# Performance work log

Hardware: AMD Instinct MI355X
Metric: run time of the kernel (lower is better)

Reference implementation:

```python
import jax, jax.numpy as jnp
import numpy as np

B, L, D, M = 8, 4096, 512, 64


def setup_inputs() -> dict:
    key = jax.random.key(0)
    k1, k2, k3 = jax.random.split(key, 3)
    scale = 1.0 / (D * D)
    return {
        "q": jax.random.normal(k1, (B, L, D), dtype=jnp.float32),
        "w_real": scale * jax.random.normal(k2, (D, D, M), dtype=jnp.float32),
        "w_imag": scale * jax.random.normal(k3, (D, D, M), dtype=jnp.float32),
    }


def reference(q, w_real, w_imag):
    # q: [B, L, D]; weights: [D, D, modes]
    b, l, d = q.shape
    n_freq = l // 2 + 1
    q_ft = jnp.fft.rfft(q, axis=1)                      # [B, n_freq, D] complex64
    m = min(w_real.shape[-1], n_freq)
    W = w_real[..., :m] + 1j * w_imag[..., :m]          # [D, E, m] complex
    # Batched over modes: replaces the per-mode python loop with one einsum.
    out_m = jnp.einsum('bmd,dem->bme', q_ft[:, :m, :], W)  # [B, m, D]
    out_ft = jnp.zeros((b, n_freq, d), dtype=q_ft.dtype).at[:, :m, :].set(out_m)
    return jnp.fft.irfft(out_ft, n=l, axis=1)           # [B, L, D] float32
```

## Files before the change

### kernel.cpp

```cpp
#include <hip/hip_runtime.h>

#define B_ 8
#define L_ 4096
#define D_ 512
#define M_ 64

typedef __attribute__((ext_vector_type(8))) short bh8;
typedef __attribute__((ext_vector_type(4))) float f4;
typedef __attribute__((ext_vector_type(4))) unsigned u32x4;

__device__ inline unsigned short f2bf(float f) {
  unsigned u = __float_as_uint(f);
  return (unsigned short)((u + 0x7fffu + ((u >> 16) & 1u)) >> 16);
}
__device__ inline unsigned packbf(float lo, float hi) {
  return (unsigned)f2bf(lo) | ((unsigned)f2bf(hi) << 16);
}

__device__ __forceinline__ void gl16(const float* g, void* l) {
  __builtin_amdgcn_global_load_lds(
      (const __attribute__((address_space(1))) unsigned*)g,
      (__attribute__((address_space(3))) unsigned*)l, 16, 0, 0);
}

__global__ void k_ftab(unsigned short* __restrict__ F) {
  int t = blockIdx.x * 256 + threadIdx.x;
  int r = t >> 12, l = t & 4095;
  int k = r & 63, part = r >> 6;
  int ph = (k * l) & (L_ - 1);
  double ang = 6.283185307179586476925286766559 * (double)ph / (double)L_;
  float v = part ? (float)(-sin(ang)) : (float)(cos(ang));
  F[t] = f2bf(v);
}

__global__ void k_gtab(unsigned short* __restrict__ G) {
  int t = blockIdx.x * 256 + threadIdx.x;
  int l = t >> 7, j = t & 127;
  int k = j & 63, part = j >> 6;
  int ph = (k * l) & (L_ - 1);
  double ang = 6.283185307179586476925286766559 * (double)ph / (double)L_;
  double ck = (k == 0 ? 1.0 : 2.0) / (double)L_;
  float v = part ? (float)(-ck * sin(ang)) : (float)(ck * cos(ang));
  G[t] = f2bf(v);
}

__global__ __launch_bounds__(512, 4) void k_dft_mfma(
    const float* __restrict__ q, const unsigned short* __restrict__ F,
    float* __restrict__ pQ) {
  int tid = threadIdx.x;
  int dt = blockIdx.x, b = blockIdx.y, kc = blockIdx.z;
  int d0 = dt * 64;
  int lbase = kc * 512;

  int w = tid >> 6, lane = tid & 63;
  int mh = w & 3, nc = w >> 2;
  int lr = lane & 15, kg = lane >> 4;

  f4 acc[2][2];
#pragma unroll
  for (int i = 0; i < 2; ++i)
#pragma unroll
    for (int j = 0; j < 2; ++j) { f4 z = {0.f, 0.f, 0.f, 0.f}; acc[i][j] = z; }

  const unsigned short* A0 = F + (size_t)(mh * 32 + lr) * 4096 + lbase + kg * 8;
  const unsigned short* A1 = A0 + (size_t)16 * 4096;
  const float* q0 = q + ((size_t)b * L_ + lbase + kg * 8) * D_ + d0 + nc * 32 + lr;

#pragma unroll 2
  for (int s = 0; s < 16; ++s) {
    const float* qs = q0 + (size_t)s * 32 * D_;
    float v0[8], v1[8];
#pragma unroll
    for (int j = 0; j < 8; ++j) {
      v0[j] = qs[(size_t)j * D_];
      v1[j] = qs[(size_t)j * D_ + 16];
    }
    union { u32x4 u; bh8 h; } bf0, bf1;
    bf0.u.x = packbf(v0[0], v0[1]); bf0.u.y = packbf(v0[2], v0[3]);
    bf0.u.z = packbf(v0[4], v0[5]); bf0.u.w = packbf(v0[6], v0[7]);
    bf1.u.x = packbf(v1[0], v1[1]); bf1.u.y = packbf(v1[2], v1[3]);
    bf1.u.z = packbf(v1[4], v1[5]); bf1.u.w = packbf(v1[6], v1[7]);
    bh8 af0 = *(const bh8*)(A0 + s * 32);
    bh8 af1 = *(const bh8*)(A1 + s * 32);
    acc[0][0] = __builtin_amdgcn_mfma_f32_16x16x32_bf16(af0, bf0.h, acc[0][0], 0, 0, 0);
    acc[0][1] = __builtin_amdgcn_mfma_f32_16x16x32_bf16(af0, bf1.h, acc[0][1], 0, 0, 0);
    acc[1][0] = __builtin_amdgcn_mfma_f32_16x16x32_bf16(af1, bf0.h, acc[1][0], 0, 0, 0);
    acc[1][1] = __builtin_amdgcn_mfma_f32_16x16x32_bf16(af1, bf1.h, acc[1][1], 0, 0, 0);
  }

#pragma unroll
  for (int mi = 0; mi < 2; ++mi) {
    int r = mh * 32 + mi * 16 + kg * 4;
#pragma unroll
    for (int ni = 0; ni < 2; ++ni) {
      int d = d0 + nc * 32 + ni * 16 + lr;
#pragma unroll
      for (int j = 0; j < 4; ++j)
        pQ[(((size_t)kc * 128 + (r + j)) * 8 + b) * 512 + d] = acc[mi][ni][j];
    }
  }
}

__global__ __launch_bounds__(256) void k_red2(const float* __restrict__ pQ,
                                              unsigned* __restrict__ Qbf) {
  int g = blockIdx.x * 256 + threadIdx.x;
  int dq = g & 127;
  int b = (g >> 7) & 7;
  int k = g >> 10;
  f4 sr = {0.f, 0.f, 0.f, 0.f}, si = {0.f, 0.f, 0.f, 0.f};
#pragma unroll
  for (int kc = 0; kc < 8; ++kc) {
    size_t base = (((size_t)kc * 128 + k) * 8 + b) * 512 + dq * 4;
    sr += *(const f4*)(pQ + base);
    si += *(const f4*)(pQ + base + (size_t)64 * 8 * 512);
  }
  u32x4 o;
  o.x = packbf(sr[0], si[0]); o.y = packbf(sr[1], si[1]);
  o.z = packbf(sr[2], si[2]); o.w = packbf(sr[3], si[3]);
  *(u32x4*)(Qbf + ((size_t)k * 8 + b) * 512 + dq * 4) = o;
}

__global__ __launch_bounds__(512, 4) void k_mix_mfma(
    const float* __restrict__ wr_, const float* __restrict__ wi_,
    const unsigned* __restrict__ Qbf, float* __restrict__ pOut) {
  __shared__ float fsr[4096];
  __shared__ float fsi[4096];
  __shared__ unsigned Wt[8192];

  int tid = threadIdx.x;
  int et = blockIdx.x, kh = blockIdx.y, dc = blockIdx.z;
  int e0 = et * 16;
  int D0 = dc * 64;
  int w = tid >> 6, lane = tid & 63;
  int er = lane & 15, kg = lane >> 4;
  int part = er >> 3, b = er & 7;
  int e8 = lane >> 3, k4g = lane & 7;

  f4 acc[4];
#pragma unroll
  for (int t = 0; t < 4; ++t) { f4 z = {0.f, 0.f, 0.f, 0.f}; acc[t] = z; }

#define GLOADW(rr, ss) do {                                                   \
    int dd_ = D0 + (rr) * 16 + (ss) * 8 + w;                                  \
    size_t gb_ = ((size_t)dd_ * 512 + e0) * 64 + kh * 32;                     \
    const float* gr_ = wr_ + gb_ + e8 * 64 + k4g * 4;                         \
    const float* gi_ = wi_ + gb_ + e8 * 64 + k4g * 4;                         \
    gl16(gr_,       (char*)fsr + (w * 2 + 0) * 1024);                         \
    gl16(gr_ + 512, (char*)fsr + (w * 2 + 1) * 1024);                         \
    gl16(gi_,       (char*)fsi + (w * 2 + 0) * 1024);                         \
    gl16(gi_ + 512, (char*)fsi + (w * 2 + 1) * 1024);                         \
  } while (0)

#define PACKW(ss) do {                                                        \
    _Pragma("unroll") for (int u = 0; u < 2; ++u) {                           \
      int cc = tid + u * 512;                                                 \
      int d_ = cc >> 7;                                                       \
      int e_ = (cc >> 3) & 15;                                                \
      int k4_ = cc & 7;                                                       \
      f4 vr = *(const f4*)&fsr[cc * 4];                                       \
      f4 vi = *(const f4*)&fsi[cc * 4];                                       \
      int dp_ = ((ss) * 8 + d_) ^ ((k4_ & 3) << 2);                           \
      int wb_ = k4_ * 1024 + e_ * 16 + dp_;                                   \
      Wt[wb_]       = packbf(vr[0], vi[0]);                                   \
      Wt[wb_ + 256] = packbf(vr[1], vi[1]);                                   \
      Wt[wb_ + 512] = packbf(vr[2], vi[2]);                                   \
      Wt[wb_ + 768] = packbf(vr[3], vi[3]);                                   \
    }                                                                         \
  } while (0)

#define COMPW(rr) do {                                                        \
    _Pragma("unroll") for (int t = 0; t < 4; ++t) {                           \
      int kl_ = w * 4 + t;                                                    \
      int sw_ = ((kl_ >> 2) & 3) << 2;                                        \
      union { u32x4 u; bh8 h; } av, bv;                                       \
      av.u = *(const u32x4*)&Wt[kl_ * 256 + er * 16 + ((kg * 4) ^ sw_)];      \
      u32x4 qv = *(const u32x4*)(Qbf +                                        \
          ((size_t)(kh * 32 + kl_) * 8 + b) * 512 + D0 + (rr) * 16 + kg * 4); \
      if (part == 0) {                                                        \
        bv.u.x = qv.x ^ 0x80000000u; bv.u.y = qv.y ^ 0x80000000u;             \
        bv.u.z = qv.z ^ 0x80000000u; bv.u.w = qv.w ^ 0x80000000u;             \
      } else {                                                                \
        bv.u.x = (qv.x >> 16) | (qv.x << 16);                                 \
        bv.u.y = (qv.y >> 16) | (qv.y << 16);                                 \
        bv.u.z = (qv.z >> 16) | (qv.z << 16);                                 \
        bv.u.w = (qv.w >> 16) | (qv.w << 16);                                 \
      }                                                                       \
      acc[t] = __builtin_amdgcn_mfma_f32_16x16x32_bf16(av.h, bv.h, acc[t], 0, 0, 0); \
    }                                                                         \
  } while (0)

  GLOADW(0, 0);
#pragma unroll 1
  for (int r = 0; r < 4; ++r) {
    __syncthreads();
    PACKW(0);
    __syncthreads();
    GLOADW(r, 1);
    __syncthreads();
    PACKW(1);
    asm volatile("s_waitcnt lgkmcnt(0)" ::: "memory");
    __builtin_amdgcn_s_barrier();
    if (r < 3) GLOADW(r + 1, 0);
    COMPW(r);
  }
#undef GLOADW
#undef PACKW
#undef COMPW

#pragma unroll
  for (int t = 0; t < 4; ++t) {
    int kglob = kh * 32 + w * 4 + t;
    size_t off = (size_t)dc * 524288 +
                 (((size_t)kglob * 2 + part) * 8 + b) * 512 + e0 + kg * 4;
    *(f4*)(pOut + off) = acc[t];
  }
}

__global__ __launch_bounds__(256) void k_psum2(const float* __restrict__ pOut,
                                               unsigned* __restrict__ Pw) {
  __shared__ float sP[128 * 33];
  int tid = threadIdx.x;
  int e0 = blockIdx.x * 32, b = blockIdx.y;
  {
    int e = tid & 31, kg4 = tid >> 5;
#pragma unroll
    for (int ii = 0; ii < 16; ++ii) {
      int col = kg4 * 16 + ii;
      int rkp = ((col & 63) << 1) | (col >> 6);
      float s = 0.f;
#pragma unroll
      for (int c = 0; c < 8; ++c)
        s += pOut[(size_t)c * 524288 + (size_t)rkp * 4096 + b * 512 + e0 + e];
      sP[col * 33 + e] = s;
    }
  }
  __syncthreads();
  {
    int e = tid >> 3, c = tid & 7;
    size_t wbase = (((size_t)b * 512 + e0 + e) * 128 + c * 16) >> 1;
#pragma unroll
    for (int ii = 0; ii < 8; ++ii) {
      int col = c * 16 + ii * 2;
      Pw[wbase + ii] = packbf(sP[col * 33 + e], sP[(col + 1) * 33 + e]);
    }
  }
}

#define LST 72
__global__ __launch_bounds__(256, 2) void k_inv_mfma(
    const short* __restrict__ G, const short* __restrict__ P,
    float* __restrict__ y) {
  __shared__ short lds[2 * 128 * LST];
  short* As = lds;
  short* Bs = lds + 128 * LST;

  int tid = threadIdx.x;
  int lt = blockIdx.x, et = blockIdx.y, b = blockIdx.z;
  int l0 = lt * 128, e0 = et * 128;

  int wv = tid >> 6, lane = tid & 63;
  int wrow = wv >> 1, wcol = wv & 1;
  int lr = lane & 15, kg = lane >> 4;

  const short* Gb = G + (size_t)l0 * 128;
  const short* Pb = P + (size_t)b * D_ * 128 + (size_t)e0 * 128;

  f4 acc[4][4];
#pragma unroll
  for (int mi = 0; mi < 4; ++mi)
#pragma unroll
    for (int ni = 0; ni < 4; ++ni) {
      f4 z = {0.f, 0.f, 0.f, 0.f};
      acc[mi][ni] = z;
    }

#pragma unroll
  for (int kh = 0; kh < 2; ++kh) {
    if (kh) __syncthreads();
#pragma unroll
    for (int i = 0; i < 4; ++i) {
      int idx = i * 256 + tid;
      int row = idx >> 3, c = idx & 7;
      *(uint4*)(As + row * LST + c * 8) =
          *(const uint4*)(Gb + (size_t)row * 128 + kh * 64 + c * 8);
      *(uint4*)(Bs + row * LST + c * 8) =
          *(const uint4*)(Pb + (size_t)row * 128 + kh * 64 + c * 8);
    }
    __syncthreads();

#pragma unroll
    for (int ks = 0; ks < 2; ++ks) {
      bh8 a[4], bf[4];
#pragma unroll
      for (int i = 0; i < 4; ++i) {
        a[i]  = *(const bh8*)(As + (wrow * 64 + i * 16 + lr) * LST + ks * 32 + kg * 8);
        bf[i] = *(const bh8*)(Bs + (wcol * 64 + i * 16 + lr) * LST + ks * 32 + kg * 8);
      }
#pragma unroll
      for (int mi = 0; mi < 4; ++mi)
#pragma unroll
        for (int ni = 0; ni < 4; ++ni)
          acc[mi][ni] = __builtin_amdgcn_mfma_f32_16x16x32_bf16(
              a[mi], bf[ni], acc[mi][ni], 0, 0, 0);
    }
  }

#pragma unroll
  for (int mi = 0; mi < 4; ++mi) {
    int lg = l0 + wrow * 64 + mi * 16 + kg * 4;
#pragma unroll
    for (int ni = 0; ni < 4; ++ni) {
      int e = e0 + wcol * 64 + ni * 16 + lr;
#pragma unroll
      for (int j = 0; j < 4; ++j)
        y[((size_t)b * L_ + (lg + j)) * D_ + e] = acc[mi][ni][j];
    }
  }
}

extern "C" void kernel_launch(void* const* d_in, const int* in_sizes, int n_in,
                              void* d_out, int out_size, void* d_ws, size_t ws_size,
                              hipStream_t stream) {
  const float* q  = (const float*)d_in[0];
  const float* wr = (const float*)d_in[1];
  const float* wi = (const float*)d_in[2];
  float* out = (float*)d_out;
  char* ws = (char*)d_ws;

  unsigned short* Fbf = (unsigned short*)ws;
  unsigned short* Gbf = (unsigned short*)(ws + (1u << 20));
  unsigned* Qbf       = (unsigned*)(ws + (2u << 20));
  unsigned* Pw        = (unsigned*)(ws + (3u << 20));

  float* pQ   = out;
  float* pOut = out;

  hipLaunchKernelGGL(k_ftab, dim3((128 * L_) / 256), dim3(256), 0, stream, Fbf);
  hipLaunchKernelGGL(k_gtab, dim3((L_ * 128) / 256), dim3(256), 0, stream, Gbf);
  hipLaunchKernelGGL(k_dft_mfma, dim3(8, 8, 8), dim3(512), 0, stream,
                     q, Fbf, pQ);
  hipLaunchKernelGGL(k_red2, dim3(65536 / 256), dim3(256), 0, stream, pQ, Qbf);
  hipLaunchKernelGGL(k_mix_mfma, dim3(32, 2, 8), dim3(512), 0, stream,
                     wr, wi, Qbf, pOut);
  hipLaunchKernelGGL(k_psum2, dim3(16, 8), dim3(256), 0, stream, pOut, Pw);
  hipLaunchKernelGGL(k_inv_mfma, dim3(L_ / 128, D_ / 128, B_), dim3(256), 0,
                     stream, (const short*)Gbf, (const short*)Pw, out);
}
```

Measured before the change: 103.3 us.

## Pipeline weight staging through four-deep async LDS ring with per-substage waits

Result: no change. 101.6 us (-1.6%).

```diff
diff --git a/kernel.cpp b/kernel.cpp
--- a/kernel.cpp
+++ b/kernel.cpp
@@ -123,88 +123,110 @@
 __global__ __launch_bounds__(512, 4) void k_mix_mfma(
     const float* __restrict__ wr_, const float* __restrict__ wi_,
     const unsigned* __restrict__ Qbf, float* __restrict__ pOut) {
-  __shared__ float fsr[4096];
-  __shared__ float fsi[4096];
+  __shared__ float fs[4][2048];
   __shared__ unsigned Wt[8192];
 
   int tid = threadIdx.x;
   int et = blockIdx.x, kh = blockIdx.y, dc = blockIdx.z;
-  int e0 = et * 16;
-  int D0 = dc * 64;
+  int e0 = et * 16, D0 = dc * 64;
   int w = tid >> 6, lane = tid & 63;
   int er = lane & 15, kg = lane >> 4;
   int part = er >> 3, b = er & 7;
+
+  int eo = w & 1, dsub = (w >> 1) & 1, arr = w >> 2;
   int e8 = lane >> 3, k4g = lane & 7;
+  const float* wlane = (arr ? wi_ : wr_) + ((size_t)(D0 + dsub) << 15) +
+                       (size_t)(e0 + eo * 8 + e8) * 64 + kh * 32 + k4g * 4;
+  float* fdst0 = &fs[0][arr * 1024 + dsub * 512 + eo * 256];
+
+  int pd = tid >> 8, pe = (tid >> 4) & 15, pk = tid & 15;
+  int psw = (pk >> 1) & 3;
+  int pbase = pd * 512 + pe * 32 + pk * 2;
+
+  const unsigned* qlane =
+      Qbf + ((size_t)(kh * 32 + w * 4) * 8 + b) * 512 + D0 + kg * 4;
 
   f4 acc[4];
 #pragma unroll
   for (int t = 0; t < 4; ++t) { f4 z = {0.f, 0.f, 0.f, 0.f}; acc[t] = z; }
-
-#define GLOADW(rr, ss) do {                                                   \
-    int dd_ = D0 + (rr) * 16 + (ss) * 8 + w;                                  \
-    size_t gb_ = ((size_t)dd_ * 512 + e0) * 64 + kh * 32;                     \
-    const float* gr_ = wr_ + gb_ + e8 * 64 + k4g * 4;                         \
-    const float* gi_ = wi_ + gb_ + e8 * 64 + k4g * 4;                         \
-    gl16(gr_,       (char*)fsr + (w * 2 + 0) * 1024);                         \
-    gl16(gr_ + 512, (char*)fsr + (w * 2 + 1) * 1024);                         \
-    gl16(gi_,       (char*)fsi + (w * 2 + 0) * 1024);                         \
-    gl16(gi_ + 512, (char*)fsi + (w * 2 + 1) * 1024);                         \
+  u32x4 qv[4];
+
+#define ISSUE(g) gl16(wlane + ((size_t)(g) << 16), fdst0 + ((g) & 3) * 2048)
+
+#define VMW(n) do { asm volatile("s_waitcnt vmcnt(" #n ")" ::: "memory"); \
+                    __builtin_amdgcn_sched_barrier(0); } while (0)
+
+#define PACKS(g) do {                                                   \
+    const float* fr_ = &fs[(g) & 3][pbase];                             \
+    float2 vr_ = *(const float2*)fr_;                                   \
+    float2 vi_ = *(const float2*)(fr_ + 1024);                          \
+    int dp_ = (((g) & 7) * 2 + pd) ^ (psw << 2);                        \
+    int wb_ = pk * 512 + pe * 16 + dp_;                                 \
+    Wt[wb_]       = packbf(vr_.x, vi_.x);                               \
+    Wt[wb_ + 256] = packbf(vr_.y, vi_.y);                               \
   } while (0)
 
-#define PACKW(ss) do {                                                        \
-    _Pragma("unroll") for (int u = 0; u < 2; ++u) {                           \
-      int cc = tid + u * 512;                                                 \
-      int d_ = cc >> 7;                                                       \
-      int e_ = (cc >> 3) & 15;                                                \
-      int k4_ = cc & 7;                                                       \
-      f4 vr = *(const f4*)&fsr[cc * 4];                                       \
-      f4 vi = *(const f4*)&fsi[cc * 4];                                       \
-      int dp_ = ((ss) * 8 + d_) ^ ((k4_ & 3) << 2);                           \
-      int wb_ = k4_ * 1024 + e_ * 16 + dp_;                                   \
-      Wt[wb_]       = packbf(vr[0], vi[0]);                                   \
-      Wt[wb_ + 256] = packbf(vr[1], vi[1]);                                   \
-      Wt[wb_ + 512] = packbf(vr[2], vi[2]);                                   \
-      Wt[wb_ + 768] = packbf(vr[3], vi[3]);                                   \
-    }                                                                         \
+#define SUBSTAGE(g, n) do {                                             \
+    VMW(n);                                                             \
+    __builtin_amdgcn_s_barrier();                                       \
+    PACKS(g);                                                           \
+    asm volatile("s_waitcnt lgkmcnt(0)" ::: "memory");                  \
+    __builtin_amdgcn_sched_barrier(0);                                  \
+    __builtin_amdgcn_s_barrier();                                       \
+    if ((g) + 4 < 32) ISSUE((g) + 4);                                   \
   } while (0)
 
-#define COMPW(rr) do {                                                        \
-    _Pragma("unroll") for (int t = 0; t < 4; ++t) {                           \
-      int kl_ = w * 4 + t;                                                    \
-      int sw_ = ((kl_ >> 2) & 3) << 2;                                        \
-      union { u32x4 u; bh8 h; } av, bv;                                       \
-      av.u = *(const u32x4*)&Wt[kl_ * 256 + er * 16 + ((kg * 4) ^ sw_)];      \
-      u32x4 qv = *(const u32x4*)(Qbf +                                        \
-          ((size_t)(kh * 32 + kl_) * 8 + b) * 512 + D0 + (rr) * 16 + kg * 4); \
-      if (part == 0) {                                                        \
-        bv.u.x = qv.x ^ 0x80000000u; bv.u.y = qv.y ^ 0x80000000u;             \
-        bv.u.z = qv.z ^ 0x80000000u; bv.u.w = qv.w ^ 0x80000000u;             \
-      } else {                                                                \
-        bv.u.x = (qv.x >> 16) | (qv.x << 16);                                 \
-        bv.u.y = (qv.y >> 16) | (qv.y << 16);                                 \
-        bv.u.z = (qv.z >> 16) | (qv.z << 16);                                 \
-        bv.u.w = (qv.w >> 16) | (qv.w << 16);                                 \
-      }                                                                       \
+#define LOADQ(r) do {                                                   \
+    _Pragma("unroll") for (int t = 0; t < 4; ++t)                       \
+      qv[t] = *(const u32x4*)(qlane + (size_t)t * 4096 + (r) * 16);     \
+    __builtin_amdgcn_sched_barrier(0);                                  \
+  } while (0)
+
+#define COMPW() do {                                                    \
+    _Pragma("unroll") for (int t = 0; t < 4; ++t) {                     \
+      int kl_ = w * 4 + t;                                              \
+      int sw_ = ((kl_ >> 2) & 3) << 2;                                  \
+      union { u32x4 u; bh8 h; } av, bv;                                 \
+      av.u = *(const u32x4*)&Wt[kl_ * 256 + er * 16 + ((kg * 4) ^ sw_)]; \
+      u32x4 q = qv[t];                                                  \
+      if (part == 0) {                                                  \
+        bv.u.x = q.x ^ 0x80000000u; bv.u.y = q.y ^ 0x80000000u;         \
+        bv.u.z = q.z ^ 0x80000000u; bv.u.w = q.w ^ 0x80000000u;         \
+      } else {                                                          \
+        bv.u.x = (q.x >> 16) | (q.x << 16); bv.u.y = (q.y >> 16) | (q.y << 16); \
+        bv.u.z = (q.z >> 16) | (q.z << 16); bv.u.w = (q.w >> 16) | (q.w << 16); \
+      }                                                                 \
       acc[t] = __builtin_amdgcn_mfma_f32_16x16x32_bf16(av.h, bv.h, acc[t], 0, 0, 0); \
-    }                                                                         \
+    }                                                                   \
   } while (0)
 
-  GLOADW(0, 0);
-#pragma unroll 1
-  for (int r = 0; r < 4; ++r) {
-    __syncthreads();
-    PACKW(0);
-    __syncthreads();
-    GLOADW(r, 1);
-    __syncthreads();
-    PACKW(1);
-    asm volatile("s_waitcnt lgkmcnt(0)" ::: "memory");
-    __builtin_amdgcn_s_barrier();
-    if (r < 3) GLOADW(r + 1, 0);
-    COMPW(r);
-  }
-#undef GLOADW
-#undef PACKW
+  ISSUE(0); ISSUE(1); ISSUE(2); ISSUE(3);
+
+  LOADQ(0);
+  SUBSTAGE(0, 7); SUBSTAGE(1, 7); SUBSTAGE(2, 7); SUBSTAGE(3, 7);
+  SUBSTAGE(4, 7); SUBSTAGE(5, 7); SUBSTAGE(6, 7); SUBSTAGE(7, 7);
+  COMPW();
+  __builtin_amdgcn_s_barrier();
+  LOADQ(1);
+  SUBSTAGE(8, 7); SUBSTAGE(9, 7); SUBSTAGE(10, 7); SUBSTAGE(11, 7);
+  SUBSTAGE(12, 7); SUBSTAGE(13, 7); SUBSTAGE(14, 7); SUBSTAGE(15, 7);
+  COMPW();
+  __builtin_amdgcn_s_barrier();
+  LOADQ(2);
+  SUBSTAGE(16, 7); SUBSTAGE(17, 7); SUBSTAGE(18, 7); SUBSTAGE(19, 7);
+  SUBSTAGE(20, 7); SUBSTAGE(21, 7); SUBSTAGE(22, 7); SUBSTAGE(23, 7);
+  COMPW();
+  __builtin_amdgcn_s_barrier();
+  LOADQ(3);
+  SUBSTAGE(24, 7); SUBSTAGE(25, 7); SUBSTAGE(26, 7); SUBSTAGE(27, 7);
+  SUBSTAGE(28, 7); SUBSTAGE(29, 6); SUBSTAGE(30, 5); SUBSTAGE(31, 4);
+  COMPW();
+
+#undef ISSUE
+#undef VMW
+#undef PACKS
+#undef SUBSTAGE
+#undef LOADQ
 #undef COMPW
 
 #pragma unroll
```
